# Optimization experiments

Hardware: AMD Instinct MI355X
Metric: run time of the kernel (lower is better)

## Reference

```python
import jax, jax.numpy as jnp
import numpy as np

B, N, DIM = 2, 2048, 256
HEADS, DHEAD = 8, 32
INNER = HEADS * DHEAD


def setup_inputs() -> dict:
    key = jax.random.key(0)
    ks = jax.random.split(key, 8)
    w = 0.05  # weight scale for numerical stability
    return {
        "x_r": jax.random.normal(ks[0], (B, N, DIM), jnp.float32),
        "x_i": jax.random.normal(ks[1], (B, N, DIM), jnp.float32),
        "Wq_r": jax.random.normal(ks[2], (INNER, DIM), jnp.float32) * w,
        "Wq_i": jax.random.normal(ks[3], (INNER, DIM), jnp.float32) * w,
        "Wkv_r": jax.random.normal(ks[4], (2 * INNER, DIM), jnp.float32) * w,
        "Wkv_i": jax.random.normal(ks[5], (2 * INNER, DIM), jnp.float32) * w,
        "Wo_r": jax.random.normal(ks[6], (DIM, INNER), jnp.float32) * w,
        "Wo_i": jax.random.normal(ks[7], (DIM, INNER), jnp.float32) * w,
    }


def _clinear(xr, xi, Wr, Wi):
    # complex linear y = x @ W^T with W as nn.Linear weight (out, in)
    yr = xr @ Wr.T - xi @ Wi.T
    yi = xr @ Wi.T + xi @ Wr.T
    return yr, yi


def _split_heads(t):  # b n (h d) -> b h n d
    b, n, hd = t.shape
    return t.reshape(b, n, HEADS, DHEAD).transpose(0, 2, 1, 3)


def reference(x_r, x_i, Wq_r, Wq_i, Wkv_r, Wkv_i, Wo_r, Wo_i):
    qr, qi = _clinear(x_r, x_i, Wq_r, Wq_i)
    kvr, kvi = _clinear(x_r, x_i, Wkv_r, Wkv_i)
    kr, vr = jnp.split(kvr, 2, axis=-1)
    ki, vi = jnp.split(kvi, 2, axis=-1)
    qr, qi, kr, ki, vr, vi = map(_split_heads, (qr, qi, kr, ki, vr, vi))

    # complete complex attention: 4 real attention passes stacked on axis r
    q_s = jnp.stack([qr, qr, qi, qi], axis=0)      # r b h n d
    k_s = jnp.stack([kr, -ki, kr, -ki], axis=0)
    v_s = jnp.stack([vr, vr, vi, vi], axis=0)

    scale = DHEAD ** -0.5
    scores = jnp.einsum('rbhnd,rbhmd->rbhnm', q_s, k_s) * scale
    attn = jax.nn.softmax(scores, axis=-1)
    out = jnp.einsum('rbhnm,rbhmd->rbhnd', attn, v_s)

    rr, ri, ir, ii = out[0], out[1], out[2], out[3]
    o_r = rr - ii
    o_i = ri + ir

    # merge heads: b h n d -> b n (h d)
    o_r = o_r.transpose(0, 2, 1, 3).reshape(B, N, INNER)
    o_i = o_i.transpose(0, 2, 1, 3).reshape(B, N, INNER)

    y_r, y_i = _clinear(o_r, o_i, Wo_r, Wo_i)
    return jnp.stack([y_r, y_i], axis=-1)  # (B, N, DIM, 2) = complex as real/imag
```

## Files before the change

### kernel.cpp

```cpp
#include <hip/hip_runtime.h>

#define SC_LOG2 0.25503486f

typedef __bf16 bf16x8 __attribute__((ext_vector_type(8)));
typedef __bf16 bf16x2 __attribute__((ext_vector_type(2)));
typedef float f32x4 __attribute__((ext_vector_type(4)));
typedef unsigned int u32x4 __attribute__((ext_vector_type(4)));

union FragU { u32x4 u; bf16x8 b; };

__device__ __forceinline__ unsigned short f2bf(float f) {
  return __builtin_bit_cast(unsigned short, (__bf16)f);
}
__device__ __forceinline__ unsigned int pkbf(float a, float b) {
  bf16x2 v = { (__bf16)a, (__bf16)b };
  return __builtin_bit_cast(unsigned int, v);
}

__device__ __forceinline__ void glds16(const void* g, void* l) {
  __builtin_amdgcn_global_load_lds(
      (const __attribute__((address_space(1))) unsigned int*)g,
      (__attribute__((address_space(3))) unsigned int*)l, 16, 0, 0);
}

__global__ __launch_bounds__(256) void prep_x(const float* __restrict__ xr,
                                              const float* __restrict__ xi,
                                              unsigned short* __restrict__ Xbf) {
  int idx = blockIdx.x * 256 + threadIdx.x;
  int m = idx >> 6;
  int c8 = (idx & 63) << 3;
  const float* src = (c8 < 256) ? (xr + (size_t)m * 256 + c8)
                                : (xi + (size_t)m * 256 + (c8 - 256));
  float4 a = *(const float4*)src;
  float4 b = *(const float4*)(src + 4);
  u32x4 o;
  o.x = pkbf(a.x, a.y);
  o.y = pkbf(a.z, a.w);
  o.z = pkbf(b.x, b.y);
  o.w = pkbf(b.z, b.w);
  *(u32x4*)(Xbf + (size_t)m * 512 + c8) = o;
}

__global__ __launch_bounds__(256) void prep_w(const float* __restrict__ Wq_r,
                                              const float* __restrict__ Wq_i,
                                              const float* __restrict__ Wkv_r,
                                              const float* __restrict__ Wkv_i,
                                              const float* __restrict__ Wo_r,
                                              const float* __restrict__ Wo_i,
                                              unsigned short* __restrict__ Wc1,
                                              unsigned short* __restrict__ Wc2) {
  int idx = blockIdx.x * 256 + threadIdx.x;
  int row = idx >> 6;
  int c8 = (idx & 63) << 3;
  bool hi = (c8 >= 256);
  int cc = hi ? (c8 - 256) : c8;
  const float* lo_p; const float* hi_p; float hsgn;
  unsigned short* dst;
  if (row < 1536) {
    int sec = row >> 8, o = row & 255;
    switch (sec) {
      case 0:  lo_p = Wq_r + (size_t)o * 256;          hi_p = Wq_i + (size_t)o * 256;          hsgn = -1.f; break;
      case 1:  lo_p = Wq_i + (size_t)o * 256;          hi_p = Wq_r + (size_t)o * 256;          hsgn =  1.f; break;
      case 2:  lo_p = Wkv_r + (size_t)o * 256;         hi_p = Wkv_i + (size_t)o * 256;         hsgn = -1.f; break;
      case 3:  lo_p = Wkv_i + (size_t)o * 256;         hi_p = Wkv_r + (size_t)o * 256;         hsgn =  1.f; break;
      case 4:  lo_p = Wkv_r + (size_t)(256 + o) * 256; hi_p = Wkv_i + (size_t)(256 + o) * 256; hsgn = -1.f; break;
      default: lo_p = Wkv_i + (size_t)(256 + o) * 256; hi_p = Wkv_r + (size_t)(256 + o) * 256; hsgn =  1.f; break;
    }
    dst = Wc1 + (size_t)row * 512 + c8;
  } else {
    int r2 = row - 1536; int comp = r2 & 1; int o = r2 >> 1;
    lo_p = comp ? (Wo_i + (size_t)o * 256) : (Wo_r + (size_t)o * 256);
    hi_p = comp ? (Wo_r + (size_t)o * 256) : (Wo_i + (size_t)o * 256);
    hsgn = comp ? 1.f : -1.f;
    dst = Wc2 + (size_t)r2 * 512 + c8;
  }
  const float* src = hi ? hi_p : lo_p;
  float sgn = hi ? hsgn : 1.f;
  if (row < 512) sgn *= SC_LOG2;
  float4 a = *(const float4*)(src + cc);
  float4 b = *(const float4*)(src + cc + 4);
  u32x4 o4;
  o4.x = pkbf(a.x * sgn, a.y * sgn);
  o4.y = pkbf(a.z * sgn, a.w * sgn);
  o4.z = pkbf(b.x * sgn, b.y * sgn);
  o4.w = pkbf(b.z * sgn, b.w * sgn);
  *(u32x4*)dst = o4;
}

__device__ __forceinline__ void gemm_main(const unsigned short* __restrict__ A,
                                          const unsigned short* __restrict__ Wm,
                                          int m0, int o0, unsigned short* lds,
                                          f32x4 (&acc)[2][2]) {
  int t = threadIdx.x;
  int lane = t & 63;
  int w = t >> 6;
  int l15 = lane & 15, g = lane >> 4;
  int sm2 = (w >> 1) * 32, sn2 = (w & 1) * 32;
  int mrow = t & 63, kg = t >> 6;
  const unsigned short* ga = A + (size_t)(m0 + mrow) * 512 + kg * 8;
  const unsigned short* gw = Wm + (size_t)(o0 + mrow) * 512 + kg * 8;
  for (int kt = 0; kt < 16; ++kt) {
    glds16(ga + kt * 32, lds + t * 8);
    glds16(gw + kt * 32, lds + 2048 + t * 8);
    __syncthreads();
    FragU a0, a1, b0, b1;
    a0.u = *(const u32x4*)(lds + g * 512 + (sm2 + l15) * 8);
    a1.u = *(const u32x4*)(lds + g * 512 + (sm2 + 16 + l15) * 8);
    b0.u = *(const u32x4*)(lds + 2048 + g * 512 + (sn2 + l15) * 8);
    b1.u = *(const u32x4*)(lds + 2048 + g * 512 + (sn2 + 16 + l15) * 8);
    acc[0][0] = __builtin_amdgcn_mfma_f32_16x16x32_bf16(a0.b, b0.b, acc[0][0], 0, 0, 0);
    acc[0][1] = __builtin_amdgcn_mfma_f32_16x16x32_bf16(a0.b, b1.b, acc[0][1], 0, 0, 0);
    acc[1][0] = __builtin_amdgcn_mfma_f32_16x16x32_bf16(a1.b, b0.b, acc[1][0], 0, 0, 0);
    acc[1][1] = __builtin_amdgcn_mfma_f32_16x16x32_bf16(a1.b, b1.b, acc[1][1], 0, 0, 0);
    __syncthreads();
  }
}

__global__ __launch_bounds__(256) void gemm_qkv(const unsigned short* __restrict__ Xbf,
                                                const unsigned short* __restrict__ Wc1,
                                                unsigned short* __restrict__ Qr,
                                                unsigned short* __restrict__ Qi,
                                                unsigned short* __restrict__ Kr,
                                                unsigned short* __restrict__ Ki,
                                                unsigned short* __restrict__ Vrt,
                                                unsigned short* __restrict__ Vit) {
  __shared__ __align__(16) unsigned short lds[4608];
  int bid = blockIdx.x;
  int m0 = (bid / 24) * 64, o0 = (bid % 24) * 64;
  f32x4 acc[2][2];
#pragma unroll
  for (int i = 0; i < 2; ++i)
#pragma unroll
    for (int j = 0; j < 2; ++j) acc[i][j] = f32x4{0.f, 0.f, 0.f, 0.f};
  gemm_main(Xbf, Wc1, m0, o0, lds, acc);
  int t = threadIdx.x;
  int lane = t & 63, w = t >> 6;
  int l15 = lane & 15, g = lane >> 4;
  int sm2 = (w >> 1) * 32, sn2 = (w & 1) * 32;
  if (o0 >= 1024) {
#pragma unroll
    for (int sm = 0; sm < 2; ++sm)
#pragma unroll
      for (int sn = 0; sn < 2; ++sn) {
        int ol = sn2 + sn * 16 + l15;
#pragma unroll
        for (int r = 0; r < 4; ++r) {
          int ml = sm2 + sm * 16 + 4 * g + r;
          lds[ol * 72 + ml] = f2bf(acc[sm][sn][r]);
        }
      }
    __syncthreads();
    int ol = t >> 2, mc = (t & 3) * 16;
    int o = o0 + ol;
    int oo = o & 255;
    int hh = oo >> 5, dd = oo & 31;
    int b = m0 >> 11, bh = b * 8 + hh;
    int n = (m0 & 2047) + mc;
    unsigned short* dst = ((o >> 8) == 4 ? Vrt : Vit) + ((size_t)bh * 32 + dd) * 2048 + n;
    u32x4 w0 = *(const u32x4*)(lds + ol * 72 + mc);
    u32x4 w1 = *(const u32x4*)(lds + ol * 72 + mc + 8);
    *(u32x4*)dst = w0;
    *(u32x4*)(dst + 8) = w1;
  } else {
#pragma unroll
    for (int sm = 0; sm < 2; ++sm)
#pragma unroll
      for (int sn = 0; sn < 2; ++sn) {
        int o = o0 + sn2 + sn * 16 + l15;
        int sec = o >> 8;
        int oo = o & 255;
        int hh = oo >> 5, dd = oo & 31;
#pragma unroll
        for (int r = 0; r < 4; ++r) {
          int m = m0 + sm2 + sm * 16 + 4 * g + r;
          int b = m >> 11, n = m & 2047;
          int bh = b * 8 + hh;
          unsigned short v = f2bf(acc[sm][sn][r]);
          switch (sec) {
            case 0:  Qr[((size_t)bh * 2048 + n) * 32 + dd] = v; break;
            case 1:  Qi[((size_t)bh * 2048 + n) * 32 + dd] = v; break;
            case 2:  Kr[((size_t)bh * 2048 + n) * 32 + dd] = v; break;
            default: Ki[((size_t)bh * 2048 + n) * 32 + dd] = v; break;
          }
        }
      }
  }
}

__global__ __launch_bounds__(256) void gemm_out(const unsigned short* __restrict__ Obf,
                                                const unsigned short* __restrict__ Wc2,
                                                float* __restrict__ out) {
  __shared__ __align__(16) unsigned short lds[4096];
  int m0 = (blockIdx.x >> 3) * 64, o0 = (blockIdx.x & 7) * 64;
  f32x4 acc[2][2];
#pragma unroll
  for (int i = 0; i < 2; ++i)
#pragma unroll
    for (int j = 0; j < 2; ++j) acc[i][j] = f32x4{0.f, 0.f, 0.f, 0.f};
  gemm_main(Obf, Wc2, m0, o0, lds, acc);
  int lane = threadIdx.x & 63, w = threadIdx.x >> 6;
  int l15 = lane & 15, g = lane >> 4;
  int sm2 = (w >> 1) * 32, sn2 = (w & 1) * 32;
#pragma unroll
  for (int sm = 0; sm < 2; ++sm)
#pragma unroll
    for (int sn = 0; sn < 2; ++sn) {
      int o = o0 + sn2 + sn * 16 + l15;
#pragma unroll
      for (int r = 0; r < 4; ++r) {
        int m = m0 + sm2 + sm * 16 + 4 * g + r;
        out[(size_t)m * 512 + o] = acc[sm][sn][r];
      }
    }
}

__global__ __launch_bounds__(256) void attn(const unsigned short* __restrict__ Qr,
                                            const unsigned short* __restrict__ Qi,
                                            const unsigned short* __restrict__ Kr,
                                            const unsigned short* __restrict__ Ki,
                                            const unsigned short* __restrict__ Vrt,
                                            const unsigned short* __restrict__ Vit,
                                            unsigned short* __restrict__ Obf) {
  __shared__ __align__(16) char smem[32768];
  unsigned short* kv = (unsigned short*)smem;

  int bid = blockIdx.x;
  int bh = bid >> 6;
  int q0 = (bid & 63) * 32;
  int t = threadIdx.x;
  int p = t >> 6, lane = t & 63;
  int l15 = lane & 15, g = lane >> 4;

  const unsigned short* Qsel = (p & 2) ? Qi : Qr;
  FragU qf[2];
#pragma unroll
  for (int s = 0; s < 2; ++s)
    qf[s].u = *(const u32x4*)(Qsel + ((size_t)bh * 2048 + q0 + s * 16 + l15) * 32 + g * 8);
  if (p & 1) {
#pragma unroll
    for (int s = 0; s < 2; ++s) qf[s].u ^= 0x80008000u;
  }

  const unsigned short* Ktile = kv + ((p & 1) ? 2048 : 0);
  const unsigned short* Vtile = kv + 4096 + ((p & 2) ? 2048 : 0);
  unsigned short* Pw = kv + 8192 + p * 2048;

  f32x4 acc[2][2];
#pragma unroll
  for (int s = 0; s < 2; ++s) { acc[s][0] = f32x4{0.f,0.f,0.f,0.f}; acc[s][1] = f32x4{0.f,0.f,0.f,0.f}; }
  float l_acc[2] = {0.f, 0.f};

  int i7 = t & 127;
  int passk = (t < 128) ? 0 : 1;
  const unsigned short* Ksrc = passk ? Ki : Kr;
  const unsigned short* Vsrc = passk ? Vit : Vrt;
  size_t kb0 = ((size_t)bh * 2048 + (i7 & 63)) * 32 + (i7 >> 6) * 8;
  size_t vb0 = ((size_t)bh * 32 + (i7 & 31)) * 2048 + (i7 >> 5) * 8;
  unsigned short* kd0 = kv + passk * 2048 + i7 * 8;
  unsigned short* vd0 = kv + 4096 + passk * 2048 + i7 * 8;

  for (int ck = 0; ck < 32; ++ck) {
    int n0 = ck * 64;
    glds16(Ksrc + kb0 + (size_t)n0 * 32, kd0);
    glds16(Ksrc + kb0 + 16 + (size_t)n0 * 32, kd0 + 1024);
    glds16(Vsrc + vb0 + n0, vd0);
    glds16(Vsrc + vb0 + 32 + n0, vd0 + 1024);
    __syncthreads();

    f32x4 st[4][2];
#pragma unroll
    for (int c = 0; c < 4; ++c) {
      FragU kf; kf.u = *(const u32x4*)(Ktile + g * 512 + (c * 16 + l15) * 8);
#pragma unroll
      for (int s = 0; s < 2; ++s)
        st[c][s] = __builtin_amdgcn_mfma_f32_16x16x32_bf16(kf.b, qf[s].b, f32x4{0.f,0.f,0.f,0.f}, 0, 0, 0);
    }

#pragma unroll
    for (int s = 0; s < 2; ++s) {
#pragma unroll
      for (int c = 0; c < 4; ++c) {
        float p0 = __builtin_amdgcn_exp2f(st[c][s][0]);
        float p1 = __builtin_amdgcn_exp2f(st[c][s][1]);
        float p2 = __builtin_amdgcn_exp2f(st[c][s][2]);
        float p3 = __builtin_amdgcn_exp2f(st[c][s][3]);
        l_acc[s] += (p0 + p1) + (p2 + p3);
        unsigned int w0 = pkbf(p0, p1);
        unsigned int w1 = pkbf(p2, p3);
        int eo = (c >> 1) * 1024 + (2 * (c & 1) + (g >> 1)) * 256 + (s * 16 + l15) * 8 + 4 * (g & 1);
        unsigned long long pv = (unsigned long long)w0 | ((unsigned long long)w1 << 32);
        *(unsigned long long*)(Pw + eo) = pv;
      }
    }

#pragma unroll
    for (int kh = 0; kh < 2; ++kh) {
      FragU vf0, vf1;
      vf0.u = *(const u32x4*)(Vtile + (4 * kh + g) * 256 + l15 * 8);
      vf1.u = *(const u32x4*)(Vtile + (4 * kh + g) * 256 + (16 + l15) * 8);
#pragma unroll
      for (int s = 0; s < 2; ++s) {
        FragU pf; pf.u = *(const u32x4*)(Pw + kh * 1024 + g * 256 + (s * 16 + l15) * 8);
        acc[s][0] = __builtin_amdgcn_mfma_f32_16x16x32_bf16(pf.b, vf0.b, acc[s][0], 0, 0, 0);
        acc[s][1] = __builtin_amdgcn_mfma_f32_16x16x32_bf16(pf.b, vf1.b, acc[s][1], 0, 0, 0);
      }
    }
    __syncthreads();
  }

  float linv[2];
#pragma unroll
  for (int s = 0; s < 2; ++s) {
    float lt = l_acc[s];
    lt += __shfl_xor(lt, 16);
    lt += __shfl_xor(lt, 32);
    linv[s] = 1.0f / lt;
  }
  float* ox = (float*)smem;
  if (p >= 2) {
    float* base = ox + ((p == 3) ? 0 : 1056);
#pragma unroll
    for (int s = 0; s < 2; ++s)
#pragma unroll
      for (int h = 0; h < 2; ++h)
#pragma unroll
        for (int r = 0; r < 4; ++r)
          base[(s * 16 + 4 * g + r) * 33 + 16 * h + l15] = acc[s][h][r] * __shfl(linv[s], 4 * g + r);
  }
  __syncthreads();
  if (p < 2) {
    const float* base = ox + ((p == 0) ? 0 : 1056);
    int coloff = (p == 0) ? 0 : 256;
    int b = bh >> 3, hh = bh & 7;
#pragma unroll
    for (int s = 0; s < 2; ++s)
#pragma unroll
      for (int h = 0; h < 2; ++h)
#pragma unroll
        for (int r = 0; r < 4; ++r) {
          float own = acc[s][h][r] * __shfl(linv[s], 4 * g + r);
          float part = base[(s * 16 + 4 * g + r) * 33 + 16 * h + l15];
          float res = (p == 0) ? (own - part) : (own + part);
          int q = q0 + s * 16 + 4 * g + r;
          Obf[((size_t)b * 2048 + q) * 512 + coloff + hh * 32 + 16 * h + l15] = f2bf(res);
        }
  }
}

extern "C" void kernel_launch(void* const* d_in, const int* in_sizes, int n_in,
                              void* d_out, int out_size, void* d_ws, size_t ws_size,
                              hipStream_t stream) {
  const float* xr    = (const float*)d_in[0];
  const float* xi    = (const float*)d_in[1];
  const float* Wq_r  = (const float*)d_in[2];
  const float* Wq_i  = (const float*)d_in[3];
  const float* Wkv_r = (const float*)d_in[4];
  const float* Wkv_i = (const float*)d_in[5];
  const float* Wo_r  = (const float*)d_in[6];
  const float* Wo_i  = (const float*)d_in[7];
  char* ws = (char*)d_ws;
  unsigned short* Xbf = (unsigned short*)(ws);
  unsigned short* Wc1 = (unsigned short*)(ws + 4194304);
  unsigned short* Wc2 = (unsigned short*)(ws + 5767168);
  unsigned short* Qr  = (unsigned short*)(ws + 6291456);
  unsigned short* Qi  = (unsigned short*)(ws + 8388608);
  unsigned short* Kr  = (unsigned short*)(ws + 10485760);
  unsigned short* Ki  = (unsigned short*)(ws + 12582912);
  unsigned short* Vrt = (unsigned short*)(ws + 14680064);
  unsigned short* Vit = (unsigned short*)(ws + 16777216);
  unsigned short* Obf = (unsigned short*)(ws + 18874368);
  float* out = (float*)d_out;

  prep_x<<<dim3(1024), dim3(256), 0, stream>>>(xr, xi, Xbf);
  prep_w<<<dim3(512), dim3(256), 0, stream>>>(Wq_r, Wq_i, Wkv_r, Wkv_i, Wo_r, Wo_i, Wc1, Wc2);
  gemm_qkv<<<dim3(1536), dim3(256), 0, stream>>>(Xbf, Wc1, Qr, Qi, Kr, Ki, Vrt, Vit);
  attn<<<dim3(1024), dim3(256), 0, stream>>>(Qr, Qi, Kr, Ki, Vrt, Vit, Obf);
  gemm_out<<<dim3(512), dim3(256), 0, stream>>>(Obf, Wc2, out);
}
```

Baseline: 185.6 us.

## Enlarge GEMM tiles and double-buffer K/V loads in attention

The QKV GEMM moves from 64x64 to 128x128 tiles and the output GEMM to 128x64 tiles, so each wave computes more MFMAs per LDS fragment load and fewer blocks are launched. The attention kernel now double-buffers its K/V tiles in LDS, prefetching the next chunk while the current one is computed, and raises wave priority around the MFMA sections. The cost is more LDS per block (48KB in attention), more registers for accumulators, and fewer blocks in the GEMMs, which could lower occupancy or leave CUs idle.

Measured after the change: 182.1 us. Within noise of the previous version (-1.9%).

```diff
diff --git a/kernel.cpp b/kernel.cpp
--- a/kernel.cpp
+++ b/kernel.cpp
@@ -87,31 +87,46 @@
   *(u32x4*)dst = o4;
 }
 
-__device__ __forceinline__ void gemm_main(const unsigned short* __restrict__ A,
-                                          const unsigned short* __restrict__ Wm,
+template<int NT>
+__device__ __forceinline__ void gemm_core(const unsigned short* __restrict__ A,
+                                          const unsigned short* __restrict__ W,
                                           int m0, int o0, unsigned short* lds,
-                                          f32x4 (&acc)[2][2]) {
+                                          f32x4 (&acc)[4][NT / 32]) {
   int t = threadIdx.x;
-  int lane = t & 63;
-  int w = t >> 6;
+  int lane = t & 63, w = t >> 6;
   int l15 = lane & 15, g = lane >> 4;
-  int sm2 = (w >> 1) * 32, sn2 = (w & 1) * 32;
-  int mrow = t & 63, kg = t >> 6;
-  const unsigned short* ga = A + (size_t)(m0 + mrow) * 512 + kg * 8;
-  const unsigned short* gw = Wm + (size_t)(o0 + mrow) * 512 + kg * 8;
+  int wm = w >> 1, wn = w & 1;
+  unsigned short* ldsB = lds + 4096;
+  const unsigned short* ga = A + (size_t)(m0 + (t & 127)) * 512 + (t >> 7) * 8;
+  const unsigned short* gw = (NT == 128)
+      ? W + (size_t)(o0 + (t & 127)) * 512 + (t >> 7) * 8
+      : W + (size_t)(o0 + (t & 63)) * 512 + (t >> 6) * 8;
   for (int kt = 0; kt < 16; ++kt) {
     glds16(ga + kt * 32, lds + t * 8);
-    glds16(gw + kt * 32, lds + 2048 + t * 8);
+    glds16(ga + 16 + kt * 32, lds + 2048 + t * 8);
+    if constexpr (NT == 128) {
+      glds16(gw + kt * 32, ldsB + t * 8);
+      glds16(gw + 16 + kt * 32, ldsB + 2048 + t * 8);
+    } else {
+      glds16(gw + kt * 32, ldsB + t * 8);
+    }
     __syncthreads();
-    FragU a0, a1, b0, b1;
-    a0.u = *(const u32x4*)(lds + g * 512 + (sm2 + l15) * 8);
-    a1.u = *(const u32x4*)(lds + g * 512 + (sm2 + 16 + l15) * 8);
-    b0.u = *(const u32x4*)(lds + 2048 + g * 512 + (sn2 + l15) * 8);
-    b1.u = *(const u32x4*)(lds + 2048 + g * 512 + (sn2 + 16 + l15) * 8);
-    acc[0][0] = __builtin_amdgcn_mfma_f32_16x16x32_bf16(a0.b, b0.b, acc[0][0], 0, 0, 0);
-    acc[0][1] = __builtin_amdgcn_mfma_f32_16x16x32_bf16(a0.b, b1.b, acc[0][1], 0, 0, 0);
-    acc[1][0] = __builtin_amdgcn_mfma_f32_16x16x32_bf16(a1.b, b0.b, acc[1][0], 0, 0, 0);
-    acc[1][1] = __builtin_amdgcn_mfma_f32_16x16x32_bf16(a1.b, b1.b, acc[1][1], 0, 0, 0);
+    FragU a[4], b[NT / 32];
+#pragma unroll
+    for (int sm = 0; sm < 4; ++sm)
+      a[sm].u = *(const u32x4*)(lds + g * 1024 + (wm * 64 + sm * 16 + l15) * 8);
+#pragma unroll
+    for (int sn = 0; sn < NT / 32; ++sn) {
+      if constexpr (NT == 128)
+        b[sn].u = *(const u32x4*)(ldsB + g * 1024 + (wn * 64 + sn * 16 + l15) * 8);
+      else
+        b[sn].u = *(const u32x4*)(ldsB + g * 512 + (wn * 32 + sn * 16 + l15) * 8);
+    }
+#pragma unroll
+    for (int sm = 0; sm < 4; ++sm)
+#pragma unroll
+      for (int sn = 0; sn < NT / 32; ++sn)
+        acc[sm][sn] = __builtin_amdgcn_mfma_f32_16x16x32_bf16(a[sm].b, b[sn].b, acc[sm][sn], 0, 0, 0);
     __syncthreads();
   }
 }
@@ -124,55 +139,59 @@
                                                 unsigned short* __restrict__ Ki,
                                                 unsigned short* __restrict__ Vrt,
                                                 unsigned short* __restrict__ Vit) {
-  __shared__ __align__(16) unsigned short lds[4608];
+  __shared__ __align__(16) unsigned short lds[8448];
   int bid = blockIdx.x;
-  int m0 = (bid / 24) * 64, o0 = (bid % 24) * 64;
-  f32x4 acc[2][2];
-#pragma unroll
-  for (int i = 0; i < 2; ++i)
-#pragma unroll
-    for (int j = 0; j < 2; ++j) acc[i][j] = f32x4{0.f, 0.f, 0.f, 0.f};
-  gemm_main(Xbf, Wc1, m0, o0, lds, acc);
+  int m0 = (bid / 12) * 128, o0 = (bid % 12) * 128;
+  f32x4 acc[4][4];
+#pragma unroll
+  for (int i = 0; i < 4; ++i)
+#pragma unroll
+    for (int j = 0; j < 4; ++j) acc[i][j] = f32x4{0.f, 0.f, 0.f, 0.f};
+  gemm_core<128>(Xbf, Wc1, m0, o0, lds, acc);
   int t = threadIdx.x;
   int lane = t & 63, w = t >> 6;
   int l15 = lane & 15, g = lane >> 4;
-  int sm2 = (w >> 1) * 32, sn2 = (w & 1) * 32;
+  int wm = w >> 1, wn = w & 1;
   if (o0 >= 1024) {
 #pragma unroll
-    for (int sm = 0; sm < 2; ++sm)
-#pragma unroll
-      for (int sn = 0; sn < 2; ++sn) {
-        int ol = sn2 + sn * 16 + l15;
-#pragma unroll
-        for (int r = 0; r < 4; ++r) {
-          int ml = sm2 + sm * 16 + 4 * g + r;
-          lds[ol * 72 + ml] = f2bf(acc[sm][sn][r]);
+    for (int h = 0; h < 2; ++h) {
+      if (wn == h) {
+#pragma unroll
+        for (int sn = 0; sn < 4; ++sn) {
+          int ol = sn * 16 + l15;
+#pragma unroll
+          for (int sm = 0; sm < 4; ++sm)
+#pragma unroll
+            for (int r = 0; r < 4; ++r)
+              lds[ol * 132 + wm * 64 + sm * 16 + 4 * g + r] = f2bf(acc[sm][sn][r]);
         }
       }
-    __syncthreads();
-    int ol = t >> 2, mc = (t & 3) * 16;
-    int o = o0 + ol;
-    int oo = o & 255;
-    int hh = oo >> 5, dd = oo & 31;
-    int b = m0 >> 11, bh = b * 8 + hh;
-    int n = (m0 & 2047) + mc;
-    unsigned short* dst = ((o >> 8) == 4 ? Vrt : Vit) + ((size_t)bh * 32 + dd) * 2048 + n;
-    u32x4 w0 = *(const u32x4*)(lds + ol * 72 + mc);
-    u32x4 w1 = *(const u32x4*)(lds + ol * 72 + mc + 8);
-    *(u32x4*)dst = w0;
-    *(u32x4*)(dst + 8) = w1;
+      __syncthreads();
+      {
+        int ol = t >> 2, mc = (t & 3) * 32;
+        int o = o0 + h * 64 + ol;
+        int oo = o & 255, dd = oo & 31, hh = oo >> 5;
+        int bh = (m0 >> 11) * 8 + hh;
+        int n = (m0 & 2047) + mc;
+        unsigned short* dstp = ((o >> 8) == 4 ? Vrt : Vit) + ((size_t)bh * 32 + dd) * 2048 + n;
+#pragma unroll
+        for (int q = 0; q < 4; ++q)
+          *(u32x4*)(dstp + q * 8) = *(const u32x4*)(lds + ol * 132 + mc + q * 8);
+      }
+      if (h == 0) __syncthreads();
+    }
   } else {
 #pragma unroll
-    for (int sm = 0; sm < 2; ++sm)
-#pragma unroll
-      for (int sn = 0; sn < 2; ++sn) {
-        int o = o0 + sn2 + sn * 16 + l15;
-        int sec = o >> 8;
-        int oo = o & 255;
-        int hh = oo >> 5, dd = oo & 31;
+    for (int sn = 0; sn < 4; ++sn) {
+      int o = o0 + wn * 64 + sn * 16 + l15;
+      int sec = o >> 8;
+      int oo = o & 255;
+      int hh = oo >> 5, dd = oo & 31;
+#pragma unroll
+      for (int sm = 0; sm < 4; ++sm)
 #pragma unroll
         for (int r = 0; r < 4; ++r) {
-          int m = m0 + sm2 + sm * 16 + 4 * g + r;
+          int m = m0 + wm * 64 + sm * 16 + 4 * g + r;
           int b = m >> 11, n = m & 2047;
           int bh = b * 8 + hh;
           unsigned short v = f2bf(acc[sm][sn][r]);
@@ -183,32 +202,32 @@
             default: Ki[((size_t)bh * 2048 + n) * 32 + dd] = v; break;
           }
         }
-      }
+    }
   }
 }
 
 __global__ __launch_bounds__(256) void gemm_out(const unsigned short* __restrict__ Obf,
                                                 const unsigned short* __restrict__ Wc2,
                                                 float* __restrict__ out) {
-  __shared__ __align__(16) unsigned short lds[4096];
-  int m0 = (blockIdx.x >> 3) * 64, o0 = (blockIdx.x & 7) * 64;
-  f32x4 acc[2][2];
-#pragma unroll
-  for (int i = 0; i < 2; ++i)
+  __shared__ __align__(16) unsigned short lds[6144];
+  int m0 = (blockIdx.x >> 3) * 128, o0 = (blockIdx.x & 7) * 64;
+  f32x4 acc[4][2];
+#pragma unroll
+  for (int i = 0; i < 4; ++i)
 #pragma unroll
     for (int j = 0; j < 2; ++j) acc[i][j] = f32x4{0.f, 0.f, 0.f, 0.f};
-  gemm_main(Obf, Wc2, m0, o0, lds, acc);
+  gemm_core<64>(Obf, Wc2, m0, o0, lds, acc);
   int lane = threadIdx.x & 63, w = threadIdx.x >> 6;
   int l15 = lane & 15, g = lane >> 4;
-  int sm2 = (w >> 1) * 32, sn2 = (w & 1) * 32;
-#pragma unroll
-  for (int sm = 0; sm < 2; ++sm)
+  int wm = w >> 1, wn = w & 1;
+#pragma unroll
+  for (int sm = 0; sm < 4; ++sm)
 #pragma unroll
     for (int sn = 0; sn < 2; ++sn) {
-      int o = o0 + sn2 + sn * 16 + l15;
+      int o = o0 + wn * 32 + sn * 16 + l15;
 #pragma unroll
       for (int r = 0; r < 4; ++r) {
-        int m = m0 + sm2 + sm * 16 + 4 * g + r;
+        int m = m0 + wm * 64 + sm * 16 + 4 * g + r;
         out[(size_t)m * 512 + o] = acc[sm][sn][r];
       }
     }
@@ -221,7 +240,7 @@
                                             const unsigned short* __restrict__ Vrt,
                                             const unsigned short* __restrict__ Vit,
                                             unsigned short* __restrict__ Obf) {
-  __shared__ __align__(16) char smem[32768];
+  __shared__ __align__(16) char smem[49152];
   unsigned short* kv = (unsigned short*)smem;
 
   int bid = blockIdx.x;
@@ -241,10 +260,6 @@
     for (int s = 0; s < 2; ++s) qf[s].u ^= 0x80008000u;
   }
 
-  const unsigned short* Ktile = kv + ((p & 1) ? 2048 : 0);
-  const unsigned short* Vtile = kv + 4096 + ((p & 2) ? 2048 : 0);
-  unsigned short* Pw = kv + 8192 + p * 2048;
-
   f32x4 acc[2][2];
 #pragma unroll
   for (int s = 0; s < 2; ++s) { acc[s][0] = f32x4{0.f,0.f,0.f,0.f}; acc[s][1] = f32x4{0.f,0.f,0.f,0.f}; }
@@ -256,18 +271,29 @@
   const unsigned short* Vsrc = passk ? Vit : Vrt;
   size_t kb0 = ((size_t)bh * 2048 + (i7 & 63)) * 32 + (i7 >> 6) * 8;
   size_t vb0 = ((size_t)bh * 32 + (i7 & 31)) * 2048 + (i7 >> 5) * 8;
-  unsigned short* kd0 = kv + passk * 2048 + i7 * 8;
-  unsigned short* vd0 = kv + 4096 + passk * 2048 + i7 * 8;
+  unsigned short* Pw = kv + 16384 + p * 2048;
+
+  auto stage = [&](int ck, int nb) {
+    int n0 = ck * 64;
+    unsigned short* kd = kv + nb * 4096 + passk * 2048 + i7 * 8;
+    unsigned short* vd = kv + 8192 + nb * 4096 + passk * 2048 + i7 * 8;
+    glds16(Ksrc + kb0 + (size_t)n0 * 32, kd);
+    glds16(Ksrc + kb0 + 16 + (size_t)n0 * 32, kd + 1024);
+    glds16(Vsrc + vb0 + n0, vd);
+    glds16(Vsrc + vb0 + 32 + n0, vd + 1024);
+  };
+
+  stage(0, 0);
+  __syncthreads();
 
   for (int ck = 0; ck < 32; ++ck) {
-    int n0 = ck * 64;
-    glds16(Ksrc + kb0 + (size_t)n0 * 32, kd0);
-    glds16(Ksrc + kb0 + 16 + (size_t)n0 * 32, kd0 + 1024);
-    glds16(Vsrc + vb0 + n0, vd0);
-    glds16(Vsrc + vb0 + 32 + n0, vd0 + 1024);
-    __syncthreads();
+    int cur = ck & 1;
+    if (ck + 1 < 32) stage(ck + 1, cur ^ 1);
+    const unsigned short* Ktile = kv + cur * 4096 + ((p & 1) ? 2048 : 0);
+    const unsigned short* Vtile = kv + 8192 + cur * 4096 + ((p & 2) ? 2048 : 0);
 
     f32x4 st[4][2];
+    __builtin_amdgcn_s_setprio(1);
 #pragma unroll
     for (int c = 0; c < 4; ++c) {
       FragU kf; kf.u = *(const u32x4*)(Ktile + g * 512 + (c * 16 + l15) * 8);
@@ -275,6 +301,7 @@
       for (int s = 0; s < 2; ++s)
         st[c][s] = __builtin_amdgcn_mfma_f32_16x16x32_bf16(kf.b, qf[s].b, f32x4{0.f,0.f,0.f,0.f}, 0, 0, 0);
     }
+    __builtin_amdgcn_s_setprio(0);
 
 #pragma unroll
     for (int s = 0; s < 2; ++s) {
@@ -293,6 +320,7 @@
       }
     }
 
+    __builtin_amdgcn_s_setprio(1);
 #pragma unroll
     for (int kh = 0; kh < 2; ++kh) {
       FragU vf0, vf1;
@@ -305,6 +333,7 @@
         acc[s][1] = __builtin_amdgcn_mfma_f32_16x16x32_bf16(pf.b, vf1.b, acc[s][1], 0, 0, 0);
       }
     }
+    __builtin_amdgcn_s_setprio(0);
     __syncthreads();
   }
 
@@ -373,7 +402,7 @@
 
   prep_x<<<dim3(1024), dim3(256), 0, stream>>>(xr, xi, Xbf);
   prep_w<<<dim3(512), dim3(256), 0, stream>>>(Wq_r, Wq_i, Wkv_r, Wkv_i, Wo_r, Wo_i, Wc1, Wc2);
-  gemm_qkv<<<dim3(1536), dim3(256), 0, stream>>>(Xbf, Wc1, Qr, Qi, Kr, Ki, Vrt, Vit);
+  gemm_qkv<<<dim3(384), dim3(256), 0, stream>>>(Xbf, Wc1, Qr, Qi, Kr, Ki, Vrt, Vit);
   attn<<<dim3(1024), dim3(256), 0, stream>>>(Qr, Qi, Kr, Ki, Vrt, Vit, Obf);
-  gemm_out<<<dim3(512), dim3(256), 0, stream>>>(Obf, Wc2, out);
-}
+  gemm_out<<<dim3(256), dim3(256), 0, stream>>>(Obf, Wc2, out);
+}
```

## Double-buffer attention K/V tiles and enlarge QKV GEMM tile to 128 rows

Applied to the files above, without the earlier changes.

The attention kernel moves from 64-key chunks with load-then-sync to 32-key chunks with a two-stage LDS double buffer, so the next tile's global-to-LDS load overlaps the current tile's MFMA and exp work. It also raises wave priority around the MFMA sections and cuts LDS use. The QKV projection GEMM now uses 128x64 tiles with 4x2 accumulators per wave, halving the grid and reusing each loaded weight tile across more rows. The cost is more loop iterations and barriers in attention, plus more registers in the GEMM.

Measured after the change: 180.5 us. 1.03x faster.

```diff
diff --git a/kernel.cpp b/kernel.cpp
--- a/kernel.cpp
+++ b/kernel.cpp
@@ -87,18 +87,114 @@
   *(u32x4*)dst = o4;
 }
 
-__device__ __forceinline__ void gemm_main(const unsigned short* __restrict__ A,
-                                          const unsigned short* __restrict__ Wm,
-                                          int m0, int o0, unsigned short* lds,
-                                          f32x4 (&acc)[2][2]) {
+__global__ __launch_bounds__(256) void gemm_qkv(const unsigned short* __restrict__ Xbf,
+                                                const unsigned short* __restrict__ Wc1,
+                                                unsigned short* __restrict__ Qr,
+                                                unsigned short* __restrict__ Qi,
+                                                unsigned short* __restrict__ Kr,
+                                                unsigned short* __restrict__ Ki,
+                                                unsigned short* __restrict__ Vrt,
+                                                unsigned short* __restrict__ Vit) {
+  __shared__ __align__(16) unsigned short lds[8448];
+  unsigned short* ldsB = lds + 4096;
+  int bid = blockIdx.x;
+  int m0 = (bid / 24) * 128, o0 = (bid % 24) * 64;
   int t = threadIdx.x;
-  int lane = t & 63;
-  int w = t >> 6;
+  int lane = t & 63, w = t >> 6;
+  int l15 = lane & 15, g = lane >> 4;
+  int wm = w >> 1, wn = w & 1;
+
+  const unsigned short* ga = Xbf + (size_t)(m0 + (t & 127)) * 512 + (t >> 7) * 8;
+  const unsigned short* gw = Wc1 + (size_t)(o0 + (t & 63)) * 512 + (t >> 6) * 8;
+
+  f32x4 acc[4][2];
+#pragma unroll
+  for (int i = 0; i < 4; ++i)
+#pragma unroll
+    for (int j = 0; j < 2; ++j) acc[i][j] = f32x4{0.f, 0.f, 0.f, 0.f};
+
+  for (int kt = 0; kt < 16; ++kt) {
+    glds16(ga + kt * 32, lds + t * 8);
+    glds16(ga + 16 + kt * 32, lds + 2048 + t * 8);
+    glds16(gw + kt * 32, ldsB + t * 8);
+    __syncthreads();
+    FragU a[4], b[2];
+#pragma unroll
+    for (int sm = 0; sm < 4; ++sm)
+      a[sm].u = *(const u32x4*)(lds + g * 1024 + (wm * 64 + sm * 16 + l15) * 8);
+#pragma unroll
+    for (int sn = 0; sn < 2; ++sn)
+      b[sn].u = *(const u32x4*)(ldsB + g * 512 + (wn * 32 + sn * 16 + l15) * 8);
+#pragma unroll
+    for (int sm = 0; sm < 4; ++sm)
+#pragma unroll
+      for (int sn = 0; sn < 2; ++sn)
+        acc[sm][sn] = __builtin_amdgcn_mfma_f32_16x16x32_bf16(a[sm].b, b[sn].b, acc[sm][sn], 0, 0, 0);
+    __syncthreads();
+  }
+
+  if (o0 >= 1024) {
+#pragma unroll
+    for (int sn = 0; sn < 2; ++sn) {
+      int ol = wn * 32 + sn * 16 + l15;
+#pragma unroll
+      for (int sm = 0; sm < 4; ++sm)
+#pragma unroll
+        for (int r = 0; r < 4; ++r)
+          lds[ol * 132 + wm * 64 + sm * 16 + 4 * g + r] = f2bf(acc[sm][sn][r]);
+    }
+    __syncthreads();
+    int ol = t >> 2, mc = (t & 3) * 32;
+    int oc = o0 + ol;
+    int oo = oc & 255, dd = oo & 31, hh = oo >> 5;
+    int bh = (m0 >> 11) * 8 + hh;
+    int n = (m0 & 2047) + mc;
+    unsigned short* dstp = ((oc >> 8) == 4 ? Vrt : Vit) + ((size_t)bh * 32 + dd) * 2048 + n;
+#pragma unroll
+    for (int q = 0; q < 4; ++q)
+      *(u32x4*)(dstp + q * 8) = *(const u32x4*)(lds + ol * 132 + mc + q * 8);
+  } else {
+#pragma unroll
+    for (int sn = 0; sn < 2; ++sn) {
+      int oc = o0 + wn * 32 + sn * 16 + l15;
+      int se = oc >> 8;
+      int oo = oc & 255;
+      int hh = oo >> 5, dd = oo & 31;
+#pragma unroll
+      for (int sm = 0; sm < 4; ++sm)
+#pragma unroll
+        for (int r = 0; r < 4; ++r) {
+          int m = m0 + wm * 64 + sm * 16 + 4 * g + r;
+          int b = m >> 11, n = m & 2047;
+          int bh = b * 8 + hh;
+          unsigned short v = f2bf(acc[sm][sn][r]);
+          switch (se) {
+            case 0:  Qr[((size_t)bh * 2048 + n) * 32 + dd] = v; break;
+            case 1:  Qi[((size_t)bh * 2048 + n) * 32 + dd] = v; break;
+            case 2:  Kr[((size_t)bh * 2048 + n) * 32 + dd] = v; break;
+            default: Ki[((size_t)bh * 2048 + n) * 32 + dd] = v; break;
+          }
+        }
+    }
+  }
+}
+
+__global__ __launch_bounds__(256) void gemm_out(const unsigned short* __restrict__ Obf,
+                                                const unsigned short* __restrict__ Wc2,
+                                                float* __restrict__ out) {
+  __shared__ __align__(16) unsigned short lds[4096];
+  int m0 = (blockIdx.x >> 3) * 64, o0 = (blockIdx.x & 7) * 64;
+  int t = threadIdx.x;
+  int lane = t & 63, w = t >> 6;
   int l15 = lane & 15, g = lane >> 4;
   int sm2 = (w >> 1) * 32, sn2 = (w & 1) * 32;
-  int mrow = t & 63, kg = t >> 6;
-  const unsigned short* ga = A + (size_t)(m0 + mrow) * 512 + kg * 8;
-  const unsigned short* gw = Wm + (size_t)(o0 + mrow) * 512 + kg * 8;
+  const unsigned short* ga = Obf + (size_t)(m0 + (t & 63)) * 512 + (t >> 6) * 8;
+  const unsigned short* gw = Wc2 + (size_t)(o0 + (t & 63)) * 512 + (t >> 6) * 8;
+  f32x4 acc[2][2];
+#pragma unroll
+  for (int i = 0; i < 2; ++i)
+#pragma unroll
+    for (int j = 0; j < 2; ++j) acc[i][j] = f32x4{0.f, 0.f, 0.f, 0.f};
   for (int kt = 0; kt < 16; ++kt) {
     glds16(ga + kt * 32, lds + t * 8);
     glds16(gw + kt * 32, lds + 2048 + t * 8);
@@ -114,93 +210,6 @@
     acc[1][1] = __builtin_amdgcn_mfma_f32_16x16x32_bf16(a1.b, b1.b, acc[1][1], 0, 0, 0);
     __syncthreads();
   }
-}
-
-__global__ __launch_bounds__(256) void gemm_qkv(const unsigned short* __restrict__ Xbf,
-                                                const unsigned short* __restrict__ Wc1,
-                                                unsigned short* __restrict__ Qr,
-                                                unsigned short* __restrict__ Qi,
-                                                unsigned short* __restrict__ Kr,
-                                                unsigned short* __restrict__ Ki,
-                                                unsigned short* __restrict__ Vrt,
-                                                unsigned short* __restrict__ Vit) {
-  __shared__ __align__(16) unsigned short lds[4608];
-  int bid = blockIdx.x;
-  int m0 = (bid / 24) * 64, o0 = (bid % 24) * 64;
-  f32x4 acc[2][2];
-#pragma unroll
-  for (int i = 0; i < 2; ++i)
-#pragma unroll
-    for (int j = 0; j < 2; ++j) acc[i][j] = f32x4{0.f, 0.f, 0.f, 0.f};
-  gemm_main(Xbf, Wc1, m0, o0, lds, acc);
-  int t = threadIdx.x;
-  int lane = t & 63, w = t >> 6;
-  int l15 = lane & 15, g = lane >> 4;
-  int sm2 = (w >> 1) * 32, sn2 = (w & 1) * 32;
-  if (o0 >= 1024) {
-#pragma unroll
-    for (int sm = 0; sm < 2; ++sm)
-#pragma unroll
-      for (int sn = 0; sn < 2; ++sn) {
-        int ol = sn2 + sn * 16 + l15;
-#pragma unroll
-        for (int r = 0; r < 4; ++r) {
-          int ml = sm2 + sm * 16 + 4 * g + r;
-          lds[ol * 72 + ml] = f2bf(acc[sm][sn][r]);
-        }
-      }
-    __syncthreads();
-    int ol = t >> 2, mc = (t & 3) * 16;
-    int o = o0 + ol;
-    int oo = o & 255;
-    int hh = oo >> 5, dd = oo & 31;
-    int b = m0 >> 11, bh = b * 8 + hh;
-    int n = (m0 & 2047) + mc;
-    unsigned short* dst = ((o >> 8) == 4 ? Vrt : Vit) + ((size_t)bh * 32 + dd) * 2048 + n;
-    u32x4 w0 = *(const u32x4*)(lds + ol * 72 + mc);
-    u32x4 w1 = *(const u32x4*)(lds + ol * 72 + mc + 8);
-    *(u32x4*)dst = w0;
-    *(u32x4*)(dst + 8) = w1;
-  } else {
-#pragma unroll
-    for (int sm = 0; sm < 2; ++sm)
-#pragma unroll
-      for (int sn = 0; sn < 2; ++sn) {
-        int o = o0 + sn2 + sn * 16 + l15;
-        int sec = o >> 8;
-        int oo = o & 255;
-        int hh = oo >> 5, dd = oo & 31;
-#pragma unroll
-        for (int r = 0; r < 4; ++r) {
-          int m = m0 + sm2 + sm * 16 + 4 * g + r;
-          int b = m >> 11, n = m & 2047;
-          int bh = b * 8 + hh;
-          unsigned short v = f2bf(acc[sm][sn][r]);
-          switch (sec) {
-            case 0:  Qr[((size_t)bh * 2048 + n) * 32 + dd] = v; break;
-            case 1:  Qi[((size_t)bh * 2048 + n) * 32 + dd] = v; break;
-            case 2:  Kr[((size_t)bh * 2048 + n) * 32 + dd] = v; break;
-            default: Ki[((size_t)bh * 2048 + n) * 32 + dd] = v; break;
-          }
-        }
-      }
-  }
-}
-
-__global__ __launch_bounds__(256) void gemm_out(const unsigned short* __restrict__ Obf,
-                                                const unsigned short* __restrict__ Wc2,
-                                                float* __restrict__ out) {
-  __shared__ __align__(16) unsigned short lds[4096];
-  int m0 = (blockIdx.x >> 3) * 64, o0 = (blockIdx.x & 7) * 64;
-  f32x4 acc[2][2];
-#pragma unroll
-  for (int i = 0; i < 2; ++i)
-#pragma unroll
-    for (int j = 0; j < 2; ++j) acc[i][j] = f32x4{0.f, 0.f, 0.f, 0.f};
-  gemm_main(Obf, Wc2, m0, o0, lds, acc);
-  int lane = threadIdx.x & 63, w = threadIdx.x >> 6;
-  int l15 = lane & 15, g = lane >> 4;
-  int sm2 = (w >> 1) * 32, sn2 = (w & 1) * 32;
 #pragma unroll
   for (int sm = 0; sm < 2; ++sm)
 #pragma unroll
@@ -221,7 +230,7 @@
                                             const unsigned short* __restrict__ Vrt,
                                             const unsigned short* __restrict__ Vit,
                                             unsigned short* __restrict__ Obf) {
-  __shared__ __align__(16) char smem[32768];
+  __shared__ __align__(16) char smem[24576];
   unsigned short* kv = (unsigned short*)smem;
 
   int bid = blockIdx.x;
@@ -241,10 +250,6 @@
     for (int s = 0; s < 2; ++s) qf[s].u ^= 0x80008000u;
   }
 
-  const unsigned short* Ktile = kv + ((p & 1) ? 2048 : 0);
-  const unsigned short* Vtile = kv + 4096 + ((p & 2) ? 2048 : 0);
-  unsigned short* Pw = kv + 8192 + p * 2048;
-
   f32x4 acc[2][2];
 #pragma unroll
   for (int s = 0; s < 2; ++s) { acc[s][0] = f32x4{0.f,0.f,0.f,0.f}; acc[s][1] = f32x4{0.f,0.f,0.f,0.f}; }
@@ -254,32 +259,40 @@
   int passk = (t < 128) ? 0 : 1;
   const unsigned short* Ksrc = passk ? Ki : Kr;
   const unsigned short* Vsrc = passk ? Vit : Vrt;
-  size_t kb0 = ((size_t)bh * 2048 + (i7 & 63)) * 32 + (i7 >> 6) * 8;
+  size_t kb0 = ((size_t)bh * 2048 + (i7 & 31)) * 32 + (i7 >> 5) * 8;
   size_t vb0 = ((size_t)bh * 32 + (i7 & 31)) * 2048 + (i7 >> 5) * 8;
-  unsigned short* kd0 = kv + passk * 2048 + i7 * 8;
-  unsigned short* vd0 = kv + 4096 + passk * 2048 + i7 * 8;
-
-  for (int ck = 0; ck < 32; ++ck) {
-    int n0 = ck * 64;
-    glds16(Ksrc + kb0 + (size_t)n0 * 32, kd0);
-    glds16(Ksrc + kb0 + 16 + (size_t)n0 * 32, kd0 + 1024);
-    glds16(Vsrc + vb0 + n0, vd0);
-    glds16(Vsrc + vb0 + 32 + n0, vd0 + 1024);
-    __syncthreads();
-
-    f32x4 st[4][2];
-#pragma unroll
-    for (int c = 0; c < 4; ++c) {
-      FragU kf; kf.u = *(const u32x4*)(Ktile + g * 512 + (c * 16 + l15) * 8);
+  unsigned short* Pw = kv + 8192 + p * 1024;
+
+  auto stage = [&](int ck, int nb) {
+    int n0 = ck * 32;
+    glds16(Ksrc + kb0 + (size_t)n0 * 32, kv + nb * 2048 + passk * 1024 + i7 * 8);
+    glds16(Vsrc + vb0 + n0, kv + 4096 + nb * 2048 + passk * 1024 + i7 * 8);
+  };
+
+  stage(0, 0);
+  __syncthreads();
+
+  for (int ck = 0; ck < 64; ++ck) {
+    int cur = ck & 1;
+    if (ck + 1 < 64) stage(ck + 1, cur ^ 1);
+    const unsigned short* Ktile = kv + cur * 2048 + ((p & 1) ? 1024 : 0);
+    const unsigned short* Vtile = kv + 4096 + cur * 2048 + ((p & 2) ? 1024 : 0);
+
+    f32x4 st[2][2];
+    __builtin_amdgcn_s_setprio(1);
+#pragma unroll
+    for (int c = 0; c < 2; ++c) {
+      FragU kf; kf.u = *(const u32x4*)(Ktile + g * 256 + (c * 16 + l15) * 8);
 #pragma unroll
       for (int s = 0; s < 2; ++s)
         st[c][s] = __builtin_amdgcn_mfma_f32_16x16x32_bf16(kf.b, qf[s].b, f32x4{0.f,0.f,0.f,0.f}, 0, 0, 0);
     }
+    __builtin_amdgcn_s_setprio(0);
 
 #pragma unroll
     for (int s = 0; s < 2; ++s) {
 #pragma unroll
-      for (int c = 0; c < 4; ++c) {
+      for (int c = 0; c < 2; ++c) {
         float p0 = __builtin_amdgcn_exp2f(st[c][s][0]);
         float p1 = __builtin_amdgcn_exp2f(st[c][s][1]);
         float p2 = __builtin_amdgcn_exp2f(st[c][s][2]);
@@ -287,24 +300,25 @@
         l_acc[s] += (p0 + p1) + (p2 + p3);
         unsigned int w0 = pkbf(p0, p1);
         unsigned int w1 = pkbf(p2, p3);
-        int eo = (c >> 1) * 1024 + (2 * (c & 1) + (g >> 1)) * 256 + (s * 16 + l15) * 8 + 4 * (g & 1);
+        int eo = (2 * c + (g >> 1)) * 256 + (s * 16 + l15) * 8 + 4 * (g & 1);
         unsigned long long pv = (unsigned long long)w0 | ((unsigned long long)w1 << 32);
         *(unsigned long long*)(Pw + eo) = pv;
       }
     }
 
-#pragma unroll
-    for (int kh = 0; kh < 2; ++kh) {
+    __builtin_amdgcn_s_setprio(1);
+    {
       FragU vf0, vf1;
-      vf0.u = *(const u32x4*)(Vtile + (4 * kh + g) * 256 + l15 * 8);
-      vf1.u = *(const u32x4*)(Vtile + (4 * kh + g) * 256 + (16 + l15) * 8);
+      vf0.u = *(const u32x4*)(Vtile + g * 256 + l15 * 8);
+      vf1.u = *(const u32x4*)(Vtile + g * 256 + (16 + l15) * 8);
 #pragma unroll
       for (int s = 0; s < 2; ++s) {
-        FragU pf; pf.u = *(const u32x4*)(Pw + kh * 1024 + g * 256 + (s * 16 + l15) * 8);
+        FragU pf; pf.u = *(const u32x4*)(Pw + g * 256 + (s * 16 + l15) * 8);
         acc[s][0] = __builtin_amdgcn_mfma_f32_16x16x32_bf16(pf.b, vf0.b, acc[s][0], 0, 0, 0);
         acc[s][1] = __builtin_amdgcn_mfma_f32_16x16x32_bf16(pf.b, vf1.b, acc[s][1], 0, 0, 0);
       }
     }
+    __builtin_amdgcn_s_setprio(0);
     __syncthreads();
   }
 
@@ -373,7 +387,7 @@
 
   prep_x<<<dim3(1024), dim3(256), 0, stream>>>(xr, xi, Xbf);
   prep_w<<<dim3(512), dim3(256), 0, stream>>>(Wq_r, Wq_i, Wkv_r, Wkv_i, Wo_r, Wo_i, Wc1, Wc2);
-  gemm_qkv<<<dim3(1536), dim3(256), 0, stream>>>(Xbf, Wc1, Qr, Qi, Kr, Ki, Vrt, Vit);
+  gemm_qkv<<<dim3(768), dim3(256), 0, stream>>>(Xbf, Wc1, Qr, Qi, Kr, Ki, Vrt, Vit);
   attn<<<dim3(1024), dim3(256), 0, stream>>>(Qr, Qi, Kr, Ki, Vrt, Vit, Obf);
   gemm_out<<<dim3(512), dim3(256), 0, stream>>>(Obf, Wc2, out);
 }
```
